# Performance work log

Hardware: AMD Instinct MI355X
Metric: run time of the kernel (lower is better)

## Reference

```python
import jax, jax.numpy as jnp
import numpy as np

N_HEADS = 16
LN_EPS = 1e-6


def _mha(q_in, kv_in, mask, wq, bq, wk, bk, wv, bv, wo, bo):
    B, Sq, D = q_in.shape
    H = N_HEADS
    dh = D // H
    def split(x):  # [B,S,D] -> [B,H,S,dh]
        return x.reshape(B, -1, H, dh).transpose(0, 2, 1, 3)
    q = split(q_in @ wq + bq)
    k = split(kv_in @ wk + bk)
    v = split(kv_in @ wv + bv)
    scores = jnp.einsum('bhqd,bhkd->bhqk', q, k) / jnp.sqrt(jnp.asarray(dh, q.dtype))
    scores = scores + mask * (-1e9)
    attn = jax.nn.softmax(scores, axis=-1)
    out = jnp.einsum('bhqk,bhkd->bhqd', attn, v)
    out = out.transpose(0, 2, 1, 3).reshape(B, Sq, D)
    return out @ wo + bo


def _layer_norm(x, gamma, beta):
    mu = jnp.mean(x, axis=-1, keepdims=True)
    var = jnp.mean(jnp.square(x - mu), axis=-1, keepdims=True)
    return (x - mu) * jax.lax.rsqrt(var + LN_EPS) * gamma + beta


def setup_inputs() -> dict:
    key = jax.random.key(0)
    B, S_dec, S_enc, D, F = 4, 1024, 1024, 1024, 4096
    ks = jax.random.split(key, 16)
    s = 0.02
    inp = {
        'inputs': jax.random.normal(ks[0], (B, S_dec, D), jnp.float32),
        'enc_outputs': jax.random.normal(ks[1], (B, S_enc, D), jnp.float32),
        # causal look-ahead mask: 1 above diagonal -> -1e9 added to scores
        'mask_1': jnp.triu(jnp.ones((S_dec, S_dec), jnp.float32), k=1)[None, None],
        'mask_2': jnp.zeros((B, 1, 1, S_enc), jnp.float32),
    }
    names = ['wq1', 'wk1', 'wv1', 'wo1', 'wq2', 'wk2', 'wv2', 'wo2']
    for i, n in enumerate(names):
        inp[n] = jax.random.normal(ks[2 + i], (D, D), jnp.float32) * s
        inp['b' + n[1:]] = jnp.zeros((D,), jnp.float32)
    inp['w_ff1'] = jax.random.normal(ks[10], (D, F), jnp.float32) * s
    inp['b_ff1'] = jnp.zeros((F,), jnp.float32)
    inp['w_ff2'] = jax.random.normal(ks[11], (F, D), jnp.float32) * s
    inp['b_ff2'] = jnp.zeros((D,), jnp.float32)
    for i in (1, 2, 3):
        inp[f'g{i}'] = jnp.ones((D,), jnp.float32)
        inp[f'beta{i}'] = jnp.zeros((D,), jnp.float32)
    return inp


def reference(inputs, enc_outputs, mask_1, mask_2,
              wq1, bq1, wk1, bk1, wv1, bv1, wo1, bo1,
              wq2, bq2, wk2, bk2, wv2, bv2, wo2, bo2,
              w_ff1, b_ff1, w_ff2, b_ff2,
              g1, beta1, g2, beta2, g3, beta3):
    # causal self-attention + residual + LN (dropout inactive at inference)
    attn = _mha(inputs, inputs, mask_1, wq1, bq1, wk1, bk1, wv1, bv1, wo1, bo1)
    attn = _layer_norm(attn + inputs, g1, beta1)
    # encoder-decoder cross-attention + residual + LN
    attn2 = _mha(attn, enc_outputs, mask_2, wq2, bq2, wk2, bk2, wv2, bv2, wo2, bo2)
    attn2 = _layer_norm(attn2 + attn, g2, beta2)
    # FFN + residual + LN
    h = jax.nn.relu(attn2 @ w_ff1 + b_ff1)
    h = h @ w_ff2 + b_ff2
    return _layer_norm(h + attn2, g3, beta3)
```

## Files before the change

kernel.cpp:

```cpp
#include <hip/hip_runtime.h>
#include <stdint.h>

typedef unsigned short ushort_t;
typedef __attribute__((ext_vector_type(8))) short bf16x8;
typedef __attribute__((ext_vector_type(4))) float f32x4;
typedef __attribute__((ext_vector_type(4))) unsigned short us4;

#define DEV __device__ __forceinline__

DEV unsigned short f2bf(float f) {
  union { float f; unsigned u; } x; x.f = f;
  unsigned r = x.u + 0x7fffu + ((x.u >> 16) & 1u);
  return (unsigned short)(r >> 16);
}

DEV void gload16(const void* g, void* l) {
  __builtin_amdgcn_global_load_lds(
      (const __attribute__((address_space(1))) unsigned int*)g,
      (__attribute__((address_space(3))) unsigned int*)l, 16, 0, 0);
}

__global__ __launch_bounds__(256) void cast_bf16_kernel(
    const float* __restrict__ x, ushort_t* __restrict__ y, int n4) {
  int i = blockIdx.x * 256 + threadIdx.x;
  if (i >= n4) return;
  float4 v = ((const float4*)x)[i];
  us4 o; o.x = f2bf(v.x); o.y = f2bf(v.y); o.z = f2bf(v.z); o.w = f2bf(v.w);
  ((us4*)y)[i] = o;
}

__global__ __launch_bounds__(256) void reduce_cast_kernel(
    const float* __restrict__ p0, const float* __restrict__ p1,
    ushort_t* __restrict__ y, int n4) {
  int i = blockIdx.x * 256 + threadIdx.x;
  if (i >= n4) return;
  float4 a = ((const float4*)p0)[i];
  float4 b = ((const float4*)p1)[i];
  us4 o; o.x = f2bf(a.x + b.x); o.y = f2bf(a.y + b.y);
  o.z = f2bf(a.z + b.z); o.w = f2bf(a.w + b.w);
  ((us4*)y)[i] = o;
}

__global__ __launch_bounds__(256) void transpose_cast_kernel(
    const float* __restrict__ W, ushort_t* __restrict__ dst, int K, int N) {
  __shared__ float tile[64][65];
  int n0 = blockIdx.x * 64, k0 = blockIdx.y * 64;
  int tid = threadIdx.x;
#pragma unroll
  for (int it = 0; it < 16; ++it) {
    int idx = it * 256 + tid; int r = idx >> 6, c = idx & 63;
    tile[r][c] = W[(size_t)(k0 + r) * N + n0 + c];
  }
  __syncthreads();
#pragma unroll
  for (int it = 0; it < 16; ++it) {
    int idx = it * 256 + tid; int r = idx >> 6, c = idx & 63;
    dst[(size_t)(n0 + r) * K + k0 + c] = f2bf(tile[c][r]);
  }
}

struct Src8 { const float* p[8]; };
__global__ __launch_bounds__(256) void transpose_cast8_kernel(
    Src8 s, ushort_t* __restrict__ dst) {
  __shared__ float tile[64][65];
  const float* W = s.p[blockIdx.z];
  ushort_t* out = dst + (size_t)blockIdx.z * 1048576;
  int n0 = blockIdx.x * 64, k0 = blockIdx.y * 64;
  int tid = threadIdx.x;
#pragma unroll
  for (int it = 0; it < 16; ++it) {
    int idx = it * 256 + tid; int r = idx >> 6, c = idx & 63;
    tile[r][c] = W[(size_t)(k0 + r) * 1024 + n0 + c];
  }
  __syncthreads();
#pragma unroll
  for (int it = 0; it < 16; ++it) {
    int idx = it * 256 + tid; int r = idx >> 6, c = idx & 63;
    out[(size_t)(n0 + r) * 1024 + k0 + c] = f2bf(tile[c][r]);
  }
}

__global__ __launch_bounds__(256) void transpose_v_kernel(
    const ushort_t* __restrict__ V, int ldv, ushort_t* __restrict__ vT) {
  __shared__ ushort_t tile[64][65];
  int s0 = blockIdx.x * 64;
  int bh = blockIdx.y;
  int b = bh >> 4, h = bh & 15;
  int tid = threadIdx.x;
#pragma unroll
  for (int it = 0; it < 4; ++it) {
    int idx = it * 256 + tid; int r = idx >> 4, c = (idx & 15) * 4;
    us4 v = *(const us4*)&V[(size_t)(b * 1024 + s0 + r) * ldv + h * 64 + c];
    tile[r][c] = v.x; tile[r][c + 1] = v.y; tile[r][c + 2] = v.z; tile[r][c + 3] = v.w;
  }
  __syncthreads();
#pragma unroll
  for (int it = 0; it < 4; ++it) {
    int idx = it * 256 + tid; int r = idx >> 4, c = (idx & 15) * 4;
    us4 o; o.x = tile[c][r]; o.y = tile[c + 1][r]; o.z = tile[c + 2][r]; o.w = tile[c + 3][r];
    *(us4*)&vT[((size_t)bh * 64 + r) * 1024 + s0 + c] = o;
  }
}

template <int WF32, int WB16, int RELU>
__global__ __launch_bounds__(256, 2) void gemm_bt(
    const ushort_t* __restrict__ A, const ushort_t* __restrict__ Bt,
    const float* __restrict__ b0, const float* __restrict__ b1,
    const float* __restrict__ b2, const float* __restrict__ b3,
    float* __restrict__ Cf, ushort_t* __restrict__ Cb,
    int M, int N, int K, int Ks, long long pstr) {
  __shared__ ushort_t sA[4096];
  __shared__ ushort_t sB[4096];
  const int tid = threadIdx.x;
  const int w = tid >> 6, lane = tid & 63;
  const int lrow = lane & 15, lk = lane >> 4;
  const int m0 = blockIdx.x * 128, n0 = blockIdx.y * 128;
  const int kz = blockIdx.z * Ks;
  const int wr = w >> 1, wc = w & 1;
  f32x4 acc[4][4] = {};
  const int brow0 = (w * 1024 + lane * 16) >> 6;
  const int kbyte = (lane * 16) & 63;

  for (int kt = kz; kt < kz + Ks; kt += 32) {
    __syncthreads();
    const ushort_t* ga = A + (size_t)(m0 + brow0) * K + kt + (kbyte >> 1);
    gload16(ga, (char*)sA + w * 1024);
    gload16(ga + (size_t)64 * K, (char*)sA + 4096 + w * 1024);
    const ushort_t* gb = Bt + (size_t)(n0 + brow0) * K + kt + (kbyte >> 1);
    gload16(gb, (char*)sB + w * 1024);
    gload16(gb + (size_t)64 * K, (char*)sB + 4096 + w * 1024);
    __syncthreads();
    bf16x8 aF[4], bF[4];
#pragma unroll
    for (int t = 0; t < 4; ++t) {
      aF[t] = *(const bf16x8*)((const char*)sA + ((wr * 64 + t * 16 + lrow) << 6) + (lk << 4));
      bF[t] = *(const bf16x8*)((const char*)sB + ((wc * 64 + t * 16 + lrow) << 6) + (lk << 4));
    }
#pragma unroll
    for (int mt = 0; mt < 4; ++mt)
#pragma unroll
      for (int nt = 0; nt < 4; ++nt)
        acc[mt][nt] = __builtin_amdgcn_mfma_f32_16x16x32_bf16(aF[mt], bF[nt], acc[mt][nt], 0, 0, 0);
  }
  float* Cfz = Cf + (long long)blockIdx.z * pstr;
#pragma unroll
  for (int nt = 0; nt < 4; ++nt) {
    int col = n0 + wc * 64 + nt * 16 + lrow;
    int seg = col >> 10;
    const float* bp = seg == 0 ? b0 : seg == 1 ? b1 : seg == 2 ? b2 : b3;
    float bv = bp[col & 1023];
    if (blockIdx.z != 0) bv = 0.f;
#pragma unroll
    for (int mt = 0; mt < 4; ++mt) {
      int rowb = m0 + wr * 64 + mt * 16 + lk * 4;
#pragma unroll
      for (int j = 0; j < 4; ++j) {
        float v = acc[mt][nt][j] + bv;
        if (RELU) v = fmaxf(v, 0.f);
        size_t idx = (size_t)(rowb + j) * N + col;
        if (WF32) Cfz[idx] = v;
        if (WB16) Cb[idx] = f2bf(v);
      }
    }
  }
}

template <int CAUSAL>
__global__ __launch_bounds__(256, 4) void attn_kernel(
    const ushort_t* __restrict__ Q, int ldq,
    const ushort_t* __restrict__ Kp, int ldk,
    const ushort_t* __restrict__ vT,
    const float* __restrict__ mask2,
    ushort_t* __restrict__ O) {
  __shared__ ushort_t sK[2][4096];
  __shared__ ushort_t sV[2][4096];
  __shared__ ushort_t sP[4][1024];
  const int bh = blockIdx.x, qb = blockIdx.y;
  const int b = bh >> 4, h = bh & 15;
  const int tid = threadIdx.x, w = tid >> 6, lane = tid & 63;
  const int lrow = lane & 15, lk = lane >> 4;

  const ushort_t* qptr = Q + (size_t)(b * 1024 + qb * 64 + w * 16 + lrow) * ldq + h * 64 + lk * 8;
  bf16x8 qF0 = *(const bf16x8*)qptr;
  bf16x8 qF1 = *(const bf16x8*)(qptr + 32);
  f32x4 oacc[4] = {};
  float m_ = -3.0e38f, l_ = 0.f;
  const int nkb = CAUSAL ? (qb + 1) : 16;
  const float C = 0.18033688011112042f;

  const int sr = w * 16 + (lane >> 3);
  const int scb = (((lane & 7) ^ (lane >> 3)) * 16);
  const ushort_t* kbase = Kp + (size_t)(b * 1024 + sr) * ldk + h * 64 + (scb >> 1);
  const ushort_t* vbase = vT + ((size_t)bh * 64 + sr) * 1024 + (scb >> 1);
  char* dstK0 = (char*)sK[0] + w * 2048;
  char* dstV0 = (char*)sV[0] + w * 2048;

#define STAGE(kb_, bufi)                                              \
  do {                                                                \
    const ushort_t* gk = kbase + (size_t)(kb_) * 64 * ldk;            \
    gload16(gk, dstK0 + (bufi) * 8192);                               \
    gload16(gk + (size_t)8 * ldk, dstK0 + (bufi) * 8192 + 1024);      \
    const ushort_t* gv = vbase + (kb_) * 64;                          \
    gload16(gv, dstV0 + (bufi) * 8192);                               \
    gload16(gv + (size_t)8 * 1024, dstV0 + (bufi) * 8192 + 1024);     \
  } while (0)

  STAGE(0, 0);
  const int swz = (lrow & 7) << 4;

  for (int kb = 0; kb < nkb; ++kb) {
    const int buf = kb & 1;
    __syncthreads();
    if (kb + 1 < nkb) STAGE(kb + 1, buf ^ 1);

    const char* kB = (const char*)sK[buf];
    const char* vB = (const char*)sV[buf];
    f32x4 sc[4];
    __builtin_amdgcn_s_setprio(1);
#pragma unroll
    for (int kt = 0; kt < 4; ++kt) {
      const char* rp = kB + ((kt * 16 + lrow) << 7);
      bf16x8 k0 = *(const bf16x8*)(rp + ((lk * 16) ^ swz));
      bf16x8 k1 = *(const bf16x8*)(rp + ((64 + lk * 16) ^ swz));
      f32x4 z = {};
      z = __builtin_amdgcn_mfma_f32_16x16x32_bf16(k0, qF0, z, 0, 0, 0);
      sc[kt] = __builtin_amdgcn_mfma_f32_16x16x32_bf16(k1, qF1, sc[kt] = z, 0, 0, 0);
    }
    __builtin_amdgcn_s_setprio(0);
    if (CAUSAL) {
      if (kb == qb) {
        int ql = w * 16 + lrow;
#pragma unroll
        for (int kt = 0; kt < 4; ++kt)
#pragma unroll
          for (int j = 0; j < 4; ++j)
            if (kt * 16 + lk * 4 + j > ql) sc[kt][j] = -3.0e38f;
      }
    } else {
#pragma unroll
      for (int kt = 0; kt < 4; ++kt) {
        float4 mv = *(const float4*)&mask2[b * 1024 + kb * 64 + kt * 16 + lk * 4];
        sc[kt][0] = fmaf(mv.x, -8e9f, sc[kt][0]);
        sc[kt][1] = fmaf(mv.y, -8e9f, sc[kt][1]);
        sc[kt][2] = fmaf(mv.z, -8e9f, sc[kt][2]);
        sc[kt][3] = fmaf(mv.w, -8e9f, sc[kt][3]);
      }
    }
    float mx = fmaxf(fmaxf(fmaxf(sc[0][0], sc[0][1]), fmaxf(sc[0][2], sc[0][3])),
                     fmaxf(fmaxf(sc[1][0], sc[1][1]), fmaxf(sc[1][2], sc[1][3])));
    mx = fmaxf(mx, fmaxf(fmaxf(fmaxf(sc[2][0], sc[2][1]), fmaxf(sc[2][2], sc[2][3])),
                         fmaxf(fmaxf(sc[3][0], sc[3][1]), fmaxf(sc[3][2], sc[3][3]))));
    mx = fmaxf(mx, __shfl_xor(mx, 16));
    mx = fmaxf(mx, __shfl_xor(mx, 32));
    float mnew = fmaxf(m_, mx);
    float scale = __builtin_exp2f((m_ - mnew) * C);
    float ps = 0.f;
#pragma unroll
    for (int kt = 0; kt < 4; ++kt)
#pragma unroll
      for (int j = 0; j < 4; ++j) {
        float e = __builtin_exp2f((sc[kt][j] - mnew) * C);
        sc[kt][j] = e;
        ps += e;
      }
    ps += __shfl_xor(ps, 16);
    ps += __shfl_xor(ps, 32);
    l_ = l_ * scale + ps;
    m_ = mnew;
    if (__any(scale < 1.f)) {
#pragma unroll
      for (int j = 0; j < 4; ++j) {
        float sj = __shfl(scale, lk * 4 + j);
        oacc[0][j] *= sj; oacc[1][j] *= sj; oacc[2][j] *= sj; oacc[3][j] *= sj;
      }
    }
    char* bp = (char*)sP[w] + lrow * 128;
#pragma unroll
    for (int kt = 0; kt < 4; ++kt) {
      unsigned d0, d1;
      asm("v_cvt_pk_bf16_f32 %0, %1, %2" : "=v"(d0) : "v"(sc[kt][0]), "v"(sc[kt][1]));
      asm("v_cvt_pk_bf16_f32 %0, %1, %2" : "=v"(d1) : "v"(sc[kt][2]), "v"(sc[kt][3]));
      uint2 dd; dd.x = d0; dd.y = d1;
      *(uint2*)(bp + ((kt * 32 + lk * 8) ^ swz)) = dd;
    }
    bf16x8 pF0 = *(const bf16x8*)(bp + ((lk * 16) ^ swz));
    bf16x8 pF1 = *(const bf16x8*)(bp + ((64 + lk * 16) ^ swz));
    __builtin_amdgcn_s_setprio(1);
#pragma unroll
    for (int t = 0; t < 4; ++t) {
      const char* rp = vB + ((t * 16 + lrow) << 7);
      bf16x8 v0 = *(const bf16x8*)(rp + ((lk * 16) ^ swz));
      bf16x8 v1 = *(const bf16x8*)(rp + ((64 + lk * 16) ^ swz));
      oacc[t] = __builtin_amdgcn_mfma_f32_16x16x32_bf16(pF0, v0, oacc[t], 0, 0, 0);
      oacc[t] = __builtin_amdgcn_mfma_f32_16x16x32_bf16(pF1, v1, oacc[t], 0, 0, 0);
    }
    __builtin_amdgcn_s_setprio(0);
  }
#undef STAGE
#pragma unroll
  for (int j = 0; j < 4; ++j) {
    float lj = __shfl(l_, lk * 4 + j);
    float invl = 1.f / lj;
    int row = qb * 64 + w * 16 + lk * 4 + j;
    ushort_t* op = O + (size_t)(b * 1024 + row) * 1024 + h * 64;
#pragma unroll
    for (int t = 0; t < 4; ++t) op[t * 16 + lrow] = f2bf(oacc[t][j] * invl);
  }
}

template <int WB16, int NPART>
__global__ __launch_bounds__(256) void ln_kernel(
    const float* __restrict__ p0, const float* __restrict__ p1,
    const float* __restrict__ p2, const float* __restrict__ p3,
    const float* __restrict__ r,
    const float* __restrict__ g, const float* __restrict__ be,
    float* __restrict__ yf, ushort_t* __restrict__ yb) {
  int row = blockIdx.x, tid = threadIdx.x;
  size_t off = (size_t)row * 1024;
  float4 va = ((const float4*)(p0 + off))[tid];
  if (NPART >= 2) {
    float4 t = ((const float4*)(p1 + off))[tid];
    va.x += t.x; va.y += t.y; va.z += t.z; va.w += t.w;
  }
  if (NPART >= 4) {
    float4 t2 = ((const float4*)(p2 + off))[tid];
    float4 t3 = ((const float4*)(p3 + off))[tid];
    va.x += t2.x + t3.x; va.y += t2.y + t3.y;
    va.z += t2.z + t3.z; va.w += t2.w + t3.w;
  }
  float4 vb = ((const float4*)(r + off))[tid];
  float x0 = va.x + vb.x, x1 = va.y + vb.y, x2 = va.z + vb.z, x3 = va.w + vb.w;
  float s = x0 + x1 + x2 + x3;
  float s2 = x0 * x0 + x1 * x1 + x2 * x2 + x3 * x3;
#pragma unroll
  for (int o = 1; o < 64; o <<= 1) { s += __shfl_xor(s, o); s2 += __shfl_xor(s2, o); }
  __shared__ float sh[8];
  if ((tid & 63) == 0) { sh[tid >> 6] = s; sh[4 + (tid >> 6)] = s2; }
  __syncthreads();
  s = sh[0] + sh[1] + sh[2] + sh[3];
  s2 = sh[4] + sh[5] + sh[6] + sh[7];
  float mu = s * 0.0009765625f;
  float var = s2 * 0.0009765625f - mu * mu;
  float inv = rsqrtf(var + 1e-6f);
  float4 gv = ((const float4*)g)[tid];
  float4 bv = ((const float4*)be)[tid];
  float y0 = (x0 - mu) * inv * gv.x + bv.x;
  float y1 = (x1 - mu) * inv * gv.y + bv.y;
  float y2 = (x2 - mu) * inv * gv.z + bv.z;
  float y3 = (x3 - mu) * inv * gv.w + bv.w;
  ((float4*)(yf + off))[tid] = make_float4(y0, y1, y2, y3);
  if (WB16) {
    us4 o; o.x = f2bf(y0); o.y = f2bf(y1); o.z = f2bf(y2); o.w = f2bf(y3);
    ((us4*)(yb + off))[tid] = o;
  }
}

extern "C" void kernel_launch(void* const* d_in, const int* in_sizes, int n_in,
                              void* d_out, int out_size, void* d_ws, size_t ws_size,
                              hipStream_t stream) {
  (void)in_sizes; (void)n_in; (void)out_size; (void)ws_size;
  const float* inputs = (const float*)d_in[0];
  const float* enc    = (const float*)d_in[1];
  const float* mask2  = (const float*)d_in[3];
  const float* wq1 = (const float*)d_in[4];  const float* bq1 = (const float*)d_in[5];
  const float* wk1 = (const float*)d_in[6];  const float* bk1 = (const float*)d_in[7];
  const float* wv1 = (const float*)d_in[8];  const float* bv1 = (const float*)d_in[9];
  const float* wo1 = (const float*)d_in[10]; const float* bo1 = (const float*)d_in[11];
  const float* wq2 = (const float*)d_in[12]; const float* bq2 = (const float*)d_in[13];
  const float* wk2 = (const float*)d_in[14]; const float* bk2 = (const float*)d_in[15];
  const float* wv2 = (const float*)d_in[16]; const float* bv2 = (const float*)d_in[17];
  const float* wo2 = (const float*)d_in[18]; const float* bo2 = (const float*)d_in[19];
  const float* wff1 = (const float*)d_in[20]; const float* bff1 = (const float*)d_in[21];
  const float* wff2 = (const float*)d_in[22]; const float* bff2 = (const float*)d_in[23];
  const float* g1 = (const float*)d_in[24]; const float* be1 = (const float*)d_in[25];
  const float* g2 = (const float*)d_in[26]; const float* be2 = (const float*)d_in[27];
  const float* g3 = (const float*)d_in[28]; const float* be3 = (const float*)d_in[29];

  char* ws = (char*)d_ws;
  const size_t MB = 1024 * 1024;
  const size_t W1M = 1048576;
  ushort_t* wt    = (ushort_t*)ws;
  ushort_t* xb    = (ushort_t*)(ws + 32 * MB);
  ushort_t* encb  = (ushort_t*)(ws + 40 * MB);
  ushort_t* qkvb  = (ushort_t*)(ws + 48 * MB);
  ushort_t* vtb   = (ushort_t*)(ws + 72 * MB);
  ushort_t* attnb = (ushort_t*)(ws + 80 * MB);
  ushort_t* y1b   = (ushort_t*)(ws + 88 * MB);
  ushort_t* y2b   = (ushort_t*)(ws + 96 * MB);
  float*    c1f   = (float*)(ws + 104 * MB);
  float*    p48f  = (float*)(ws + 48 * MB);
  float*    y1f   = (float*)(ws + 120 * MB);
  float*    y2f   = (float*)(ws + 136 * MB);
  ushort_t* q2b   = (ushort_t*)(ws + 32 * MB);
  ushort_t* kv2b  = (ushort_t*)(ws + 56 * MB);
  ushort_t* hb    = (ushort_t*)(ws + 32 * MB);
  float*    pff   = (float*)(ws + 72 * MB);
  float* outf = (float*)d_out;
  const long long PELEMS = 4 * 1024 * 1024;
  const long long P48OFF = (long long)(p48f - c1f);

  cast_bf16_kernel<<<4096, 256, 0, stream>>>(inputs, xb, 1048576);
  cast_bf16_kernel<<<4096, 256, 0, stream>>>(enc, encb, 1048576);
  Src8 s8; s8.p[0] = wq1; s8.p[1] = wk1; s8.p[2] = wv1; s8.p[3] = wo1;
           s8.p[4] = wq2; s8.p[5] = wk2; s8.p[6] = wv2; s8.p[7] = wo2;
  transpose_cast8_kernel<<<dim3(16, 16, 8), 256, 0, stream>>>(s8, wt);
  transpose_cast_kernel<<<dim3(64, 16), 256, 0, stream>>>(wff1, wt + 8 * W1M, 1024, 4096);
  transpose_cast_kernel<<<dim3(16, 64), 256, 0, stream>>>(wff2, wt + 12 * W1M, 4096, 1024);

  gemm_bt<0, 1, 0><<<dim3(32, 24, 1), 256, 0, stream>>>(
      xb, wt, bq1, bk1, bv1, bv1, nullptr, qkvb, 4096, 3072, 1024, 1024, 0);
  transpose_v_kernel<<<dim3(16, 64), 256, 0, stream>>>(qkvb + 2048, 3072, vtb);
  attn_kernel<1><<<dim3(64, 16), 256, 0, stream>>>(
      qkvb, 3072, qkvb + 1024, 3072, vtb, nullptr, attnb);
  gemm_bt<1, 0, 0><<<dim3(32, 8, 2), 256, 0, stream>>>(
      attnb, wt + 3 * W1M, bo1, bo1, bo1, bo1, c1f, nullptr, 4096, 1024, 1024, 512, P48OFF);
  ln_kernel<1, 2><<<4096, 256, 0, stream>>>(c1f, p48f, nullptr, nullptr,
                                            inputs, g1, be1, y1f, y1b);

  gemm_bt<1, 0, 0><<<dim3(32, 8, 2), 256, 0, stream>>>(
      y1b, wt + 4 * W1M, bq2, bq2, bq2, bq2, c1f, nullptr, 4096, 1024, 1024, 512, P48OFF);
  reduce_cast_kernel<<<4096, 256, 0, stream>>>(c1f, p48f, q2b, 1048576);
  gemm_bt<0, 1, 0><<<dim3(32, 16, 1), 256, 0, stream>>>(
      encb, wt + 5 * W1M, bk2, bv2, bk2, bk2, nullptr, kv2b, 4096, 2048, 1024, 1024, 0);
  transpose_v_kernel<<<dim3(16, 64), 256, 0, stream>>>(kv2b + 1024, 2048, vtb);
  attn_kernel<0><<<dim3(64, 16), 256, 0, stream>>>(
      q2b, 1024, kv2b, 2048, vtb, mask2, attnb);
  gemm_bt<1, 0, 0><<<dim3(32, 8, 2), 256, 0, stream>>>(
      attnb, wt + 7 * W1M, bo2, bo2, bo2, bo2, c1f, nullptr, 4096, 1024, 1024, 512, P48OFF);
  ln_kernel<1, 2><<<4096, 256, 0, stream>>>(c1f, p48f, nullptr, nullptr,
                                            y1f, g2, be2, y2f, y2b);

  gemm_bt<0, 1, 1><<<dim3(32, 32, 1), 256, 0, stream>>>(
      y2b, wt + 8 * W1M, bff1, bff1 + 1024, bff1 + 2048, bff1 + 3072,
      nullptr, hb, 4096, 4096, 1024, 1024, 0);
  gemm_bt<1, 0, 0><<<dim3(32, 8, 4), 256, 0, stream>>>(
      hb, wt + 12 * W1M, bff2, bff2, bff2, bff2, pff, nullptr,
      4096, 1024, 4096, 1024, PELEMS);
  ln_kernel<0, 4><<<4096, 256, 0, stream>>>(pff, pff + PELEMS, pff + 2 * PELEMS,
                                            pff + 3 * PELEMS, y2f, g3, be3, outf, nullptr);
}
```

Baseline: 373.1 us.

## Add 256x256-tile pipelined GEMM kernel for QKV and FFN projections

Adds a new 512-thread GEMM kernel with 256x256 output tiles, a double-buffered 128KB LDS ring filled by direct global-to-LDS loads, XOR-swizzled LDS layout, and a four-phase per-tile schedule that interleaves staging with MFMA bursts under priority hints and explicit vmcnt waits. It replaces the 128x128 gemm_bt for the fused QKV projection and both FFN GEMMs, aiming to raise arithmetic intensity per LDS byte and hide global load latency. The larger tiles lower block counts (e.g. 192 or 256 blocks), which risks under-filling the GPU's CUs and wave quantization, and the heavy register footprint may limit occupancy.

Result: slower. 381.8 us (+2.3%).

```diff
diff --git a/kernel.cpp b/kernel.cpp
--- a/kernel.cpp
+++ b/kernel.cpp
@@ -19,6 +19,8 @@
       (const __attribute__((address_space(1))) unsigned int*)g,
       (__attribute__((address_space(3))) unsigned int*)l, 16, 0, 0);
 }
+
+#define MFMA16 __builtin_amdgcn_mfma_f32_16x16x32_bf16
 
 __global__ __launch_bounds__(256) void cast_bf16_kernel(
     const float* __restrict__ x, ushort_t* __restrict__ y, int n4) {
@@ -140,7 +142,7 @@
     for (int mt = 0; mt < 4; ++mt)
 #pragma unroll
       for (int nt = 0; nt < 4; ++nt)
-        acc[mt][nt] = __builtin_amdgcn_mfma_f32_16x16x32_bf16(aF[mt], bF[nt], acc[mt][nt], 0, 0, 0);
+        acc[mt][nt] = MFMA16(aF[mt], bF[nt], acc[mt][nt], 0, 0, 0);
   }
   float* Cfz = Cf + (long long)blockIdx.z * pstr;
 #pragma unroll
@@ -156,6 +158,146 @@
 #pragma unroll
       for (int j = 0; j < 4; ++j) {
         float v = acc[mt][nt][j] + bv;
+        if (RELU) v = fmaxf(v, 0.f);
+        size_t idx = (size_t)(rowb + j) * N + col;
+        if (WF32) Cfz[idx] = v;
+        if (WB16) Cb[idx] = f2bf(v);
+      }
+    }
+  }
+}
+
+template <int WF32, int WB16, int RELU>
+__global__ __launch_bounds__(512, 2) void gemm256(
+    const ushort_t* __restrict__ A, const ushort_t* __restrict__ Bt,
+    const float* __restrict__ b0, const float* __restrict__ b1,
+    const float* __restrict__ b2, const float* __restrict__ b3,
+    float* __restrict__ Cf, ushort_t* __restrict__ Cb,
+    int M, int N, int K, int Ks, long long pstr) {
+  extern __shared__ char L[];
+  const int tid = threadIdx.x;
+  const int w = tid >> 6, lane = tid & 63;
+  const int lrow = lane & 15, lk = lane >> 4;
+  const int wm = w >> 2, wn = w & 3;
+  const int m0 = blockIdx.x * 256, n0 = blockIdx.y * 256;
+  const int kz = blockIdx.z * Ks;
+  const int nt = Ks >> 6;
+
+  const int rL = lane >> 2;
+  const int csw = (lane & 3) ^ (rL & 3);
+  const ushort_t* srcA = A + (size_t)(m0 + w * 16 + rL) * K + kz + csw * 8;
+  const ushort_t* srcB = Bt + (size_t)(n0 + w * 16 + rL) * K + kz + csw * 8;
+  const int dstw = w * 1024;
+
+#define STG(M_, KK_, T_)                                                      \
+  do {                                                                        \
+    const ushort_t* g0 = ((M_) ? srcB : srcA) + (size_t)(T_) * 64 + (KK_) * 32; \
+    char* d_ = L + (((T_) & 1) << 16) + ((M_) << 15) + ((KK_) << 14) + dstw;  \
+    gload16(g0, d_);                                                          \
+    gload16(g0 + (size_t)128 * K, d_ + 8192);                                 \
+  } while (0)
+
+  f32x4 acc[8][4] = {};
+  const int lkx16 = (lk ^ (lrow & 3)) << 4;
+  const int arow = (wm * 128 + lrow) << 6;
+  const int brow = (wn * 64 + lrow) << 6;
+
+  STG(0, 0, 0); STG(1, 0, 0); STG(0, 1, 0); STG(1, 1, 0);
+  STG(0, 0, 1); STG(1, 0, 1); STG(0, 1, 1);
+  asm volatile("s_waitcnt vmcnt(6)" ::: "memory");
+  __builtin_amdgcn_s_barrier();
+
+  for (int t = 0; t < nt; ++t) {
+    const int buf = (t & 1) << 16;
+    bf16x8 aF[8], bF0, bF1;
+    {
+      const char* pA = L + buf + arow + lkx16;
+#pragma unroll
+      for (int m = 0; m < 8; ++m) aF[m] = *(const bf16x8*)(pA + m * 1024);
+      const char* pB = L + buf + 32768 + brow + lkx16;
+      bF0 = *(const bf16x8*)pB;
+      bF1 = *(const bf16x8*)(pB + 1024);
+      if (t + 1 < nt) STG(1, 1, t + 1);
+      __builtin_amdgcn_s_barrier();
+      __builtin_amdgcn_s_setprio(1);
+#pragma unroll
+      for (int m = 0; m < 8; ++m) {
+        acc[m][0] = MFMA16(aF[m], bF0, acc[m][0], 0, 0, 0);
+        acc[m][1] = MFMA16(aF[m], bF1, acc[m][1], 0, 0, 0);
+      }
+      __builtin_amdgcn_s_setprio(0);
+      __builtin_amdgcn_s_barrier();
+    }
+    {
+      const char* pB = L + buf + 32768 + brow + lkx16;
+      bF0 = *(const bf16x8*)(pB + 2048);
+      bF1 = *(const bf16x8*)(pB + 3072);
+      if (t + 2 < nt) STG(0, 0, t + 2);
+      __builtin_amdgcn_s_barrier();
+      __builtin_amdgcn_s_setprio(1);
+#pragma unroll
+      for (int m = 0; m < 8; ++m) {
+        acc[m][2] = MFMA16(aF[m], bF0, acc[m][2], 0, 0, 0);
+        acc[m][3] = MFMA16(aF[m], bF1, acc[m][3], 0, 0, 0);
+      }
+      __builtin_amdgcn_s_setprio(0);
+      __builtin_amdgcn_s_barrier();
+    }
+    {
+      const char* pA = L + buf + 16384 + arow + lkx16;
+#pragma unroll
+      for (int m = 0; m < 8; ++m) aF[m] = *(const bf16x8*)(pA + m * 1024);
+      const char* pB = L + buf + 32768 + 16384 + brow + lkx16;
+      bF0 = *(const bf16x8*)pB;
+      bF1 = *(const bf16x8*)(pB + 1024);
+      if (t + 2 < nt) STG(1, 0, t + 2);
+      __builtin_amdgcn_s_barrier();
+      __builtin_amdgcn_s_setprio(1);
+#pragma unroll
+      for (int m = 0; m < 8; ++m) {
+        acc[m][0] = MFMA16(aF[m], bF0, acc[m][0], 0, 0, 0);
+        acc[m][1] = MFMA16(aF[m], bF1, acc[m][1], 0, 0, 0);
+      }
+      __builtin_amdgcn_s_setprio(0);
+      __builtin_amdgcn_s_barrier();
+    }
+    {
+      const char* pB = L + buf + 32768 + 16384 + brow + lkx16;
+      bF0 = *(const bf16x8*)(pB + 2048);
+      bF1 = *(const bf16x8*)(pB + 3072);
+      if (t + 2 < nt) {
+        STG(0, 1, t + 2);
+        asm volatile("s_waitcnt vmcnt(6)" ::: "memory");
+      } else {
+        asm volatile("s_waitcnt vmcnt(0)" ::: "memory");
+      }
+      __builtin_amdgcn_s_barrier();
+      __builtin_amdgcn_s_setprio(1);
+#pragma unroll
+      for (int m = 0; m < 8; ++m) {
+        acc[m][2] = MFMA16(aF[m], bF0, acc[m][2], 0, 0, 0);
+        acc[m][3] = MFMA16(aF[m], bF1, acc[m][3], 0, 0, 0);
+      }
+      __builtin_amdgcn_s_setprio(0);
+      __builtin_amdgcn_s_barrier();
+    }
+  }
+#undef STG
+
+  float* Cfz = Cf + (long long)blockIdx.z * pstr;
+#pragma unroll
+  for (int n = 0; n < 4; ++n) {
+    int col = n0 + wn * 64 + n * 16 + lrow;
+    int seg = col >> 10;
+    const float* bp = seg == 0 ? b0 : seg == 1 ? b1 : seg == 2 ? b2 : b3;
+    float bv = bp[col & 1023];
+    if (blockIdx.z != 0) bv = 0.f;
+#pragma unroll
+    for (int m = 0; m < 8; ++m) {
+      int rowb = m0 + wm * 128 + m * 16 + lk * 4;
+#pragma unroll
+      for (int j = 0; j < 4; ++j) {
+        float v = acc[m][n][j] + bv;
         if (RELU) v = fmaxf(v, 0.f);
         size_t idx = (size_t)(rowb + j) * N + col;
         if (WF32) Cfz[idx] = v;
@@ -223,8 +365,8 @@
       bf16x8 k0 = *(const bf16x8*)(rp + ((lk * 16) ^ swz));
       bf16x8 k1 = *(const bf16x8*)(rp + ((64 + lk * 16) ^ swz));
       f32x4 z = {};
-      z = __builtin_amdgcn_mfma_f32_16x16x32_bf16(k0, qF0, z, 0, 0, 0);
-      sc[kt] = __builtin_amdgcn_mfma_f32_16x16x32_bf16(k1, qF1, sc[kt] = z, 0, 0, 0);
+      z = MFMA16(k0, qF0, z, 0, 0, 0);
+      sc[kt] = MFMA16(k1, qF1, z, 0, 0, 0);
     }
     __builtin_amdgcn_s_setprio(0);
     if (CAUSAL) {
@@ -291,8 +433,8 @@
       const char* rp = vB + ((t * 16 + lrow) << 7);
       bf16x8 v0 = *(const bf16x8*)(rp + ((lk * 16) ^ swz));
       bf16x8 v1 = *(const bf16x8*)(rp + ((64 + lk * 16) ^ swz));
-      oacc[t] = __builtin_amdgcn_mfma_f32_16x16x32_bf16(pF0, v0, oacc[t], 0, 0, 0);
-      oacc[t] = __builtin_amdgcn_mfma_f32_16x16x32_bf16(pF1, v1, oacc[t], 0, 0, 0);
+      oacc[t] = MFMA16(pF0, v0, oacc[t], 0, 0, 0);
+      oacc[t] = MFMA16(pF1, v1, oacc[t], 0, 0, 0);
     }
     __builtin_amdgcn_s_setprio(0);
   }
@@ -407,7 +549,7 @@
   transpose_cast_kernel<<<dim3(64, 16), 256, 0, stream>>>(wff1, wt + 8 * W1M, 1024, 4096);
   transpose_cast_kernel<<<dim3(16, 64), 256, 0, stream>>>(wff2, wt + 12 * W1M, 4096, 1024);
 
-  gemm_bt<0, 1, 0><<<dim3(32, 24, 1), 256, 0, stream>>>(
+  gemm256<0, 1, 0><<<dim3(16, 12, 1), 512, 131072, stream>>>(
       xb, wt, bq1, bk1, bv1, bv1, nullptr, qkvb, 4096, 3072, 1024, 1024, 0);
   transpose_v_kernel<<<dim3(16, 64), 256, 0, stream>>>(qkvb + 2048, 3072, vtb);
   attn_kernel<1><<<dim3(64, 16), 256, 0, stream>>>(
@@ -430,10 +572,10 @@
   ln_kernel<1, 2><<<4096, 256, 0, stream>>>(c1f, p48f, nullptr, nullptr,
                                             y1f, g2, be2, y2f, y2b);
 
-  gemm_bt<0, 1, 1><<<dim3(32, 32, 1), 256, 0, stream>>>(
+  gemm256<0, 1, 1><<<dim3(16, 16, 1), 512, 131072, stream>>>(
       y2b, wt + 8 * W1M, bff1, bff1 + 1024, bff1 + 2048, bff1 + 3072,
       nullptr, hb, 4096, 4096, 1024, 1024, 0);
-  gemm_bt<1, 0, 0><<<dim3(32, 8, 4), 256, 0, stream>>>(
+  gemm256<1, 0, 0><<<dim3(16, 4, 4), 512, 131072, stream>>>(
       hb, wt + 12 * W1M, bff2, bff2, bff2, bff2, pff, nullptr,
       4096, 1024, 4096, 1024, PELEMS);
   ln_kernel<0, 4><<<4096, 256, 0, stream>>>(pff, pff + PELEMS, pff + 2 * PELEMS,
```
